# Optimization experiments

Hardware: AMD Instinct MI355X
Metric: run time of the kernel (lower is better)

## Reference

```python
import jax, jax.numpy as jnp
import numpy as np

B, LIMG, LTXT = 1, 2048, 256
H, NH, HD = 3072, 24, 128
MLP = int(H * 4.0)
EPS = 1e-6


def setup_inputs() -> dict:
    key = jax.random.key(0)
    ks = iter(jax.random.split(key, 64))
    rn = lambda shape, s=0.02: jax.random.normal(next(ks), shape, jnp.float32) * s
    inp = {
        'img': jax.random.normal(next(ks), (B, LIMG, H), jnp.float32),
        'txt': jax.random.normal(next(ks), (B, LTXT, H), jnp.float32),
        'vec': jax.random.normal(next(ks), (B, H), jnp.float32),
        'pe': jax.random.normal(next(ks), (1, 1, LTXT + LIMG, HD // 2, 2, 2), jnp.float32),
    }
    for p in ('img', 'txt'):
        inp[f'{p}_mod_w'] = rn((H, 6 * H)); inp[f'{p}_mod_b'] = jnp.zeros((6 * H,), jnp.float32)
        inp[f'{p}_ln1_s'] = jnp.ones((H,), jnp.float32); inp[f'{p}_ln1_b'] = jnp.zeros((H,), jnp.float32)
        inp[f'{p}_qkv_w'] = rn((H, 3 * H)); inp[f'{p}_qkv_b'] = jnp.zeros((3 * H,), jnp.float32)
        inp[f'{p}_qn'] = jnp.ones((HD,), jnp.float32); inp[f'{p}_kn'] = jnp.ones((HD,), jnp.float32)
        inp[f'{p}_proj_w'] = rn((H, H)); inp[f'{p}_proj_b'] = jnp.zeros((H,), jnp.float32)
        inp[f'{p}_ln2_s'] = jnp.ones((H,), jnp.float32); inp[f'{p}_ln2_b'] = jnp.zeros((H,), jnp.float32)
        inp[f'{p}_mlp_w1'] = rn((H, MLP)); inp[f'{p}_mlp_b1'] = jnp.zeros((MLP,), jnp.float32)
        inp[f'{p}_mlp_w2'] = rn((MLP, H)); inp[f'{p}_mlp_b2'] = jnp.zeros((H,), jnp.float32)
    return inp


def _ln(x, s, b):
    m = jnp.mean(x, -1, keepdims=True)
    v = jnp.mean((x - m) ** 2, -1, keepdims=True)
    return (x - m) * jax.lax.rsqrt(v + EPS) * s + b


def _rms(x, s):
    return x * jax.lax.rsqrt(jnp.mean(x * x, -1, keepdims=True) + EPS) * s


def _apply_rope(x, pe):
    # x: (B,NH,L,HD); pe: (1,1,L,HD/2,2,2)
    xr = x.reshape(*x.shape[:-1], HD // 2, 1, 2)
    out = pe[..., 0] * xr[..., 0] + pe[..., 1] * xr[..., 1]  # (B,NH,L,HD/2,2)
    return out.reshape(x.shape)


def _attention(q, k, v, pe):
    q = _apply_rope(q, pe)
    k = _apply_rope(k, pe)
    scores = jnp.einsum('bhqd,bhkd->bhqk', q, k) / jnp.sqrt(jnp.float32(HD))
    a = jax.nn.softmax(scores, axis=-1)
    x = jnp.einsum('bhqk,bhkd->bhqd', a, v)  # (B,NH,L,HD)
    return x.transpose(0, 2, 1, 3).reshape(x.shape[0], x.shape[2], NH * HD)


def _mod(vec, w, b):
    o = jnp.dot(jax.nn.silu(vec), w) + b          # (B, 6H)
    return jnp.split(o[:, None, :], 6, axis=-1)


def _qkv_heads(x, w, b, qn, kn):
    Bx, L, _ = x.shape
    qkv = (jnp.dot(x, w) + b).reshape(Bx, L, 3, NH, HD).transpose(2, 0, 3, 1, 4)
    q, k, v = qkv[0], qkv[1], qkv[2]
    return _rms(q, qn), _rms(k, kn), v


def reference(img, txt, vec, pe,
              img_mod_w, img_mod_b, img_ln1_s, img_ln1_b, img_qkv_w, img_qkv_b,
              img_qn, img_kn, img_proj_w, img_proj_b, img_ln2_s, img_ln2_b,
              img_mlp_w1, img_mlp_b1, img_mlp_w2, img_mlp_b2,
              txt_mod_w, txt_mod_b, txt_ln1_s, txt_ln1_b, txt_qkv_w, txt_qkv_b,
              txt_qn, txt_kn, txt_proj_w, txt_proj_b, txt_ln2_s, txt_ln2_b,
              txt_mlp_w1, txt_mlp_b1, txt_mlp_w2, txt_mlp_b2):
    i_sh1, i_sc1, i_g1, i_sh2, i_sc2, i_g2 = _mod(vec, img_mod_w, img_mod_b)
    t_sh1, t_sc1, t_g1, t_sh2, t_sc2, t_g2 = _mod(vec, txt_mod_w, txt_mod_b)

    img_mod = (1 + i_sc1) * _ln(img, img_ln1_s, img_ln1_b) + i_sh1
    txt_mod = (1 + t_sc1) * _ln(txt, txt_ln1_s, txt_ln1_b) + t_sh1

    iq, ik, iv = _qkv_heads(img_mod, img_qkv_w, img_qkv_b, img_qn, img_kn)
    tq, tk, tv = _qkv_heads(txt_mod, txt_qkv_w, txt_qkv_b, txt_qn, txt_kn)

    q = jnp.concatenate([tq, iq], axis=2)
    k = jnp.concatenate([tk, ik], axis=2)
    v = jnp.concatenate([tv, iv], axis=2)
    attn = _attention(q, k, v, pe)  # (B, Ltxt+Limg, H)
    Lt = txt.shape[1]
    txt_attn, img_attn = attn[:, :Lt], attn[:, Lt:]

    img = img + i_g1 * (jnp.dot(img_attn, img_proj_w) + img_proj_b)
    h = (1 + i_sc2) * _ln(img, img_ln2_s, img_ln2_b) + i_sh2
    img = img + i_g2 * (jnp.dot(jax.nn.gelu(jnp.dot(h, img_mlp_w1) + img_mlp_b1), img_mlp_w2) + img_mlp_b2)

    txt = txt + t_g1 * (jnp.dot(txt_attn, txt_proj_w) + txt_proj_b)
    h = (1 + t_sc2) * _ln(txt, txt_ln2_s, txt_ln2_b) + t_sh2
    txt = txt + t_g2 * (jnp.dot(jax.nn.gelu(jnp.dot(h, txt_mlp_w1) + txt_mlp_b1), txt_mlp_w2) + txt_mlp_b2)
    return (img, txt)
```

## Files before the change

### kernel.cpp

```cpp
#include <hip/hip_runtime.h>
#include <hip/hip_bf16.h>
#include <cstdint>

typedef __attribute__((ext_vector_type(8))) short s16x8;
typedef __attribute__((ext_vector_type(4))) short s16x4;
typedef __attribute__((ext_vector_type(2))) short s16x2;
typedef __attribute__((ext_vector_type(4))) float f32x4;

#define LTXT 256
#define LIMG 2048
#define LTOT 2304
#define HDIM 3072
#define NHEADS 24
#define HD 128
#define MLPD 12288

__device__ __forceinline__ short f2bf(float f) {
  union { float f; uint32_t u; } v; v.f = f;
  uint32_t r = v.u + 0x7FFFu + ((v.u >> 16) & 1u);
  return (short)(r >> 16);
}
__device__ __forceinline__ float bf2f(short s) {
  union { uint32_t u; float f; } v; v.u = ((uint32_t)(uint16_t)s) << 16;
  return v.f;
}

#define GLDS16(gsrc, ldst)                                                   \
  __builtin_amdgcn_global_load_lds(                                          \
      (const __attribute__((address_space(1))) uint32_t*)(gsrc),             \
      (__attribute__((address_space(3))) uint32_t*)(ldst), 16, 0, 0)

__global__ __launch_bounds__(256)
void wconv(const float* __restrict__ Wf, short* __restrict__ Wt, int K, int N)
{
  __shared__ short Ls[64][68];
  const int t = threadIdx.x;
  const int k0 = blockIdx.x * 64, n0 = blockIdx.y * 64;
  #pragma unroll
  for (int rep = 0; rep < 4; ++rep) {
    int idx = rep * 256 + t;
    int k = idx >> 4;
    int n = (idx & 15) * 4;
    float4 v = *(const float4*)(Wf + (size_t)(k0 + k) * N + n0 + n);
    Ls[k][n + 0] = f2bf(v.x); Ls[k][n + 1] = f2bf(v.y);
    Ls[k][n + 2] = f2bf(v.z); Ls[k][n + 3] = f2bf(v.w);
  }
  __syncthreads();
  #pragma unroll
  for (int rep = 0; rep < 4; ++rep) {
    int idx = rep * 256 + t;
    int n = idx >> 4;
    int k = (idx & 15) * 4;
    s16x4 o = { Ls[k + 0][n], Ls[k + 1][n], Ls[k + 2][n], Ls[k + 3][n] };
    *(s16x4*)(Wt + (size_t)(n0 + n) * K + k0 + k) = o;
  }
}

__global__ __launch_bounds__(256)
void mod_gemv(const float* __restrict__ vec,
              const float* __restrict__ w_img, const float* __restrict__ b_img,
              const float* __restrict__ w_txt, const float* __restrict__ b_txt,
              float* __restrict__ mod_img, float* __restrict__ mod_txt)
{
  __shared__ float sv[HDIM];
  const int t = threadIdx.x;
  for (int i = t; i < HDIM; i += 256) {
    float x = vec[i];
    sv[i] = x / (1.f + __expf(-x));
  }
  __syncthreads();
  const float* w = blockIdx.y ? w_txt : w_img;
  const float* bb = blockIdx.y ? b_txt : b_img;
  float* o = blockIdx.y ? mod_txt : mod_img;
  const int lane = t & 63, kc = t >> 6;
  const int colbase = blockIdx.x * 256 + lane * 4;
  f32x4 acc = {0.f, 0.f, 0.f, 0.f};
  const float* wp = w + (size_t)kc * 768 * 18432 + colbase;
  #pragma unroll 4
  for (int k = 0; k < 768; ++k) {
    float4 wv = *(const float4*)wp;
    float s = sv[kc * 768 + k];
    acc[0] += s * wv.x; acc[1] += s * wv.y;
    acc[2] += s * wv.z; acc[3] += s * wv.w;
    wp += 18432;
  }
  __shared__ f32x4 part[4][64];
  part[kc][lane] = acc;
  __syncthreads();
  if (t < 64) {
    f32x4 r = part[0][t];
    #pragma unroll
    for (int c = 1; c < 4; ++c) r += part[c][t];
    int cb = blockIdx.x * 256 + t * 4;
    float4 bv = *(const float4*)(bb + cb);
    float4 ov; ov.x = r[0] + bv.x; ov.y = r[1] + bv.y;
    ov.z = r[2] + bv.z; ov.w = r[3] + bv.w;
    *(float4*)(o + cb) = ov;
  }
}

__global__ __launch_bounds__(256)
void ln_mod(const float* __restrict__ xi, const float* __restrict__ xt, int rows_img,
            const float* __restrict__ si, const float* __restrict__ bi,
            const float* __restrict__ st, const float* __restrict__ bt,
            const float* __restrict__ modi, const float* __restrict__ modt,
            int sh_chunk, int sc_chunk,
            short* __restrict__ oi, short* __restrict__ ot)
{
  const int row = blockIdx.x;
  const float *x, *s, *b, *mod;
  short* out;
  if (row < rows_img) {
    x = xi + (size_t)row * HDIM; s = si; b = bi; mod = modi;
    out = oi + (size_t)row * HDIM;
  } else {
    int lr = row - rows_img;
    x = xt + (size_t)lr * HDIM; s = st; b = bt; mod = modt;
    out = ot + (size_t)lr * HDIM;
  }
  const float* sh = mod + (size_t)sh_chunk * HDIM;
  const float* sc = mod + (size_t)sc_chunk * HDIM;
  const int t = threadIdx.x;
  float xv[12];
  {
    float4 a = *(const float4*)(x + t * 12 + 0);
    float4 c = *(const float4*)(x + t * 12 + 4);
    float4 d = *(const float4*)(x + t * 12 + 8);
    xv[0]=a.x; xv[1]=a.y; xv[2]=a.z; xv[3]=a.w;
    xv[4]=c.x; xv[5]=c.y; xv[6]=c.z; xv[7]=c.w;
    xv[8]=d.x; xv[9]=d.y; xv[10]=d.z; xv[11]=d.w;
  }
  float sum = 0.f, ss = 0.f;
  #pragma unroll
  for (int e = 0; e < 12; ++e) { sum += xv[e]; ss += xv[e] * xv[e]; }
  for (int xm = 1; xm < 64; xm <<= 1) {
    sum += __shfl_xor(sum, xm);
    ss  += __shfl_xor(ss, xm);
  }
  __shared__ float red[8];
  const int w = t >> 6, lane = t & 63;
  if (lane == 0) { red[w] = sum; red[4 + w] = ss; }
  __syncthreads();
  sum = red[0] + red[1] + red[2] + red[3];
  ss  = red[4] + red[5] + red[6] + red[7];
  const float mean = sum * (1.f / HDIM);
  const float var = ss * (1.f / HDIM) - mean * mean;
  const float rs = rsqrtf(var + 1e-6f);
  short ov[12];
  #pragma unroll
  for (int e = 0; e < 12; ++e) {
    int c = t * 12 + e;
    float y = (xv[e] - mean) * rs * s[c] + b[c];
    ov[e] = f2bf((1.f + sc[c]) * y + sh[c]);
  }
  #pragma unroll
  for (int j = 0; j < 3; ++j) {
    s16x4 v = { ov[j*4+0], ov[j*4+1], ov[j*4+2], ov[j*4+3] };
    *(s16x4*)(out + t * 12 + j * 4) = v;
  }
}

template<int EPI>
__global__ __launch_bounds__(512, 2)
void gemm256(const short* __restrict__ A, int K, int N, int split,
             const short* __restrict__ W0, const short* __restrict__ W1,
             const float* __restrict__ b0, const float* __restrict__ b1,
             void* __restrict__ out0, void* __restrict__ out1,
             const float* __restrict__ r0, const float* __restrict__ r1,
             const float* __restrict__ g0, const float* __restrict__ g1)
{
  __shared__ __align__(16) short lds[65536];
  const int tid = threadIdx.x;
  const int lane = tid & 63, w = tid >> 6;
  const int wm = w >> 2, wn = w & 3;
  const int l15 = lane & 15, lg = lane >> 4;

  const int gx = gridDim.x;
  const int nwg = gx * gridDim.y;
  const int lin = blockIdx.y * gx + blockIdx.x;
  const int q8 = nwg >> 3, r8 = nwg & 7;
  const int xcd = lin & 7, loc = lin >> 3;
  const int nid = (xcd < r8 ? xcd * (q8 + 1) : r8 * (q8 + 1) + (xcd - r8) * q8) + loc;
  const int bm = nid % gx, bn = nid / gx;

  const bool is1 = bm >= split;
  const int m0 = bm * 256, n0 = bn * 256;
  const short* WT = is1 ? W1 : W0;
  const float* bias = is1 ? b1 : b0;
  const int nt = K >> 6;

  f32x4 acc[8][4];
  #pragma unroll
  for (int i = 0; i < 8; ++i)
    #pragma unroll
    for (int j = 0; j < 4; ++j)
      acc[i][j] = f32x4{0.f, 0.f, 0.f, 0.f};

  auto stage_item = [&](const short* mat, int grow0, int tt, int kh, int ldsOff) {
    const int kb = tt * 64 + kh * 32;
    #pragma unroll
    for (int l = 0; l < 2; ++l) {
      const int chrow = w * 32 + l * 16 + (lane >> 2);
      const int lc = (lane & 3) ^ ((chrow >> 1) & 3);
      GLDS16(mat + (size_t)(grow0 + chrow) * K + kb + lc * 8,
             lds + ldsOff + (w * 2 + l) * 512);
    }
  };

  const int rA0 = wm * 128 + l15;
  const int rB0 = wn * 64 + l15;
  const int cofs = (lg ^ ((l15 >> 1) & 3)) * 8;

  s16x8 av[4], bv[4];
  auto ldA4 = [&](int c, int ks, int mfb) {
    const short* base = lds + c * 32768 + ks * 8192;
    #pragma unroll
    for (int i = 0; i < 4; ++i)
      av[i] = *(const s16x8*)(base + (rA0 + (mfb + i) * 16) * 32 + cofs);
  };
  auto ldB4 = [&](int c, int ks) {
    const short* base = lds + c * 32768 + 16384 + ks * 8192;
    #pragma unroll
    for (int i = 0; i < 4; ++i)
      bv[i] = *(const s16x8*)(base + (rB0 + i * 16) * 32 + cofs);
  };
  auto quad = [&](int mfb) {
    __builtin_amdgcn_s_setprio(1);
    #pragma unroll
    for (int i = 0; i < 4; ++i)
      #pragma unroll
      for (int j = 0; j < 4; ++j)
        acc[mfb + i][j] = __builtin_amdgcn_mfma_f32_16x16x32_bf16(
            av[i], bv[j], acc[mfb + i][j], 0, 0, 0);
    __builtin_amdgcn_s_setprio(0);
  };

  stage_item(A, m0, 0, 0, 0);
  stage_item(WT, n0, 0, 0, 16384);
  stage_item(A, m0, 0, 1, 8192);
  stage_item(WT, n0, 0, 1, 24576);
  if (nt > 1) {
    stage_item(A, m0, 1, 0, 32768);
    stage_item(WT, n0, 1, 0, 49152);
  }
  asm volatile("s_waitcnt vmcnt(8)" ::: "memory");
  __builtin_amdgcn_s_barrier();
  __builtin_amdgcn_sched_barrier(0);

  for (int t = 0; t < nt; ++t) {
    const int c = t & 1;
    const int cb = c * 32768, cnb = (c ^ 1) * 32768;
    ldA4(c, 0, 0);
    ldB4(c, 0);
    if (t + 1 < nt) stage_item(A, m0, t + 1, 1, cnb + 8192);
    __builtin_amdgcn_s_barrier();
    __builtin_amdgcn_sched_barrier(0);
    quad(0);
    __builtin_amdgcn_s_barrier();
    __builtin_amdgcn_sched_barrier(0);
    ldA4(c, 0, 4);
    if (t + 1 < nt) {
      stage_item(WT, n0, t + 1, 1, cnb + 24576);
      asm volatile("s_waitcnt vmcnt(8)" ::: "memory");
    } else {
      asm volatile("s_waitcnt vmcnt(0)" ::: "memory");
    }
    __builtin_amdgcn_s_barrier();
    __builtin_amdgcn_sched_barrier(0);
    quad(4);
    __builtin_amdgcn_s_barrier();
    __builtin_amdgcn_sched_barrier(0);
    ldA4(c, 1, 0);
    ldB4(c, 1);
    if (t + 2 < nt) stage_item(A, m0, t + 2, 0, cb);
    __builtin_amdgcn_s_barrier();
    __builtin_amdgcn_sched_barrier(0);
    quad(0);
    __builtin_amdgcn_s_barrier();
    __builtin_amdgcn_sched_barrier(0);
    ldA4(c, 1, 4);
    if (t + 2 < nt) {
      stage_item(WT, n0, t + 2, 0, cb + 16384);
      asm volatile("s_waitcnt vmcnt(8)" ::: "memory");
    } else if (t + 1 < nt) {
      asm volatile("s_waitcnt vmcnt(4)" ::: "memory");
    }
    __builtin_amdgcn_s_barrier();
    __builtin_amdgcn_sched_barrier(0);
    quad(4);
    __builtin_amdgcn_s_barrier();
    __builtin_amdgcn_sched_barrier(0);
  }

  const int lrbase = m0 - (is1 ? split * 256 : 0);
  #pragma unroll
  for (int mf = 0; mf < 8; ++mf)
    #pragma unroll
    for (int nf = 0; nf < 4; ++nf) {
      int col = n0 + wn * 64 + nf * 16 + l15;
      float bvs = bias[col];
      #pragma unroll
      for (int r = 0; r < 4; ++r) {
        int row = lrbase + wm * 128 + mf * 16 + lg * 4 + r;
        float x = acc[mf][nf][r] + bvs;
        if constexpr (EPI == 0) {
          short* o = (short*)(is1 ? out1 : out0);
          o[(size_t)row * N + col] = f2bf(x);
        } else if constexpr (EPI == 1) {
          float g = 0.5f * x * (1.f + tanhf(0.7978845608028654f * (x + 0.044715f * x * x * x)));
          short* o = (short*)(is1 ? out1 : out0);
          o[(size_t)row * N + col] = f2bf(g);
        } else if constexpr (EPI == 2) {
          const float* resid = is1 ? r1 : r0;
          const float* gate = is1 ? g1 : g0;
          float* o = (float*)(is1 ? out1 : out0);
          o[(size_t)row * N + col] = resid[(size_t)row * N + col] + gate[col] * x;
        } else {
          const float* gate = is1 ? g1 : g0;
          float* o = (float*)(is1 ? out1 : out0);
          size_t ix = (size_t)row * N + col;
          o[ix] = o[ix] + gate[col] * x;
        }
      }
    }
}

__global__ __launch_bounds__(256)
void qkvr(const short* __restrict__ qkv, const float* __restrict__ pe,
          const float* __restrict__ qn_img, const float* __restrict__ kn_img,
          const float* __restrict__ qn_txt, const float* __restrict__ kn_txt,
          short* __restrict__ Qh, short* __restrict__ Kh)
{
  const int w = threadIdx.x >> 6, lane = threadIdx.x & 63;
  const int tok = blockIdx.x * 4 + w;
  const int h = blockIdx.y;
  const float* qn = (tok < LTXT) ? qn_txt : qn_img;
  const float* kn = (tok < LTXT) ? kn_txt : kn_img;
  const size_t base = (size_t)tok * 9216 + (size_t)h * HD + lane * 2;
  const float4 p4 = *(const float4*)(pe + ((size_t)tok * 64 + lane) * 4);
  {
    s16x2 qs = *(const s16x2*)(qkv + base);
    float x0 = bf2f(qs[0]), x1 = bf2f(qs[1]);
    float sq = x0 * x0 + x1 * x1;
    for (int xm = 1; xm < 64; xm <<= 1) sq += __shfl_xor(sq, xm);
    float r = rsqrtf(sq * (1.f / HD) + 1e-6f);
    x0 = x0 * r * qn[lane * 2]; x1 = x1 * r * qn[lane * 2 + 1];
    s16x2 o = { f2bf(p4.x * x0 + p4.y * x1), f2bf(p4.z * x0 + p4.w * x1) };
    *(s16x2*)(Qh + ((size_t)h * LTOT + tok) * HD + lane * 2) = o;
  }
  {
    s16x2 ks = *(const s16x2*)(qkv + base + HDIM);
    float x0 = bf2f(ks[0]), x1 = bf2f(ks[1]);
    float sq = x0 * x0 + x1 * x1;
    for (int xm = 1; xm < 64; xm <<= 1) sq += __shfl_xor(sq, xm);
    float r = rsqrtf(sq * (1.f / HD) + 1e-6f);
    x0 = x0 * r * kn[lane * 2]; x1 = x1 * r * kn[lane * 2 + 1];
    s16x2 o = { f2bf(p4.x * x0 + p4.y * x1), f2bf(p4.z * x0 + p4.w * x1) };
    *(s16x2*)(Kh + ((size_t)h * LTOT + tok) * HD + lane * 2) = o;
  }
}

__global__ __launch_bounds__(256)
void vt_k(const short* __restrict__ qkv, short* __restrict__ VT)
{
  __shared__ __align__(16) short Vs[64][136];
  const int h = blockIdx.y, tok0 = blockIdx.x * 64;
  const int t = threadIdx.x;
  #pragma unroll
  for (int rep = 0; rep < 4; ++rep) {
    int idx = rep * 256 + t;
    int tk = idx >> 4, oct = idx & 15;
    *(s16x8*)(&Vs[tk][oct * 8]) =
        *(const s16x8*)(qkv + (size_t)(tok0 + tk) * 9216 + 6144 + (size_t)h * HD + oct * 8);
  }
  __syncthreads();
  #pragma unroll
  for (int rep = 0; rep < 4; ++rep) {
    int idx = rep * 256 + t;
    int d = idx >> 3, tg = idx & 7;
    s16x8 o;
    #pragma unroll
    for (int j = 0; j < 8; ++j) o[j] = Vs[tg * 8 + j][d];
    *(s16x8*)(VT + ((size_t)h * HD + d) * LTOT + tok0 + tg * 8) = o;
  }
}

__global__ __launch_bounds__(256, 2)
void attn_k(const short* __restrict__ Qh, const short* __restrict__ Kh,
            const short* __restrict__ VT, short* __restrict__ out)
{
  __shared__ __align__(16) short Ps[4][32][72];
  const int t = threadIdx.x, lane = t & 63, w = t >> 6;
  const int l15 = lane & 15, lg = lane >> 4;
  const int h = blockIdx.y;
  const int qrow = blockIdx.x * 128 + w * 32;

  s16x8 qf[2][4];
  #pragma unroll
  for (int mf = 0; mf < 2; ++mf)
    #pragma unroll
    for (int ks = 0; ks < 4; ++ks)
      qf[mf][ks] = *(const s16x8*)(Qh + ((size_t)h * LTOT + qrow + mf * 16 + l15) * HD + ks * 32 + lg * 8);

  f32x4 O[2][8];
  #pragma unroll
  for (int mf = 0; mf < 2; ++mf)
    #pragma unroll
    for (int dt = 0; dt < 8; ++dt) O[mf][dt] = f32x4{0.f, 0.f, 0.f, 0.f};
  float mrow[2][4], lrow[2][4];
  #pragma unroll
  for (int mf = 0; mf < 2; ++mf)
    #pragma unroll
    for (int r = 0; r < 4; ++r) { mrow[mf][r] = -1e30f; lrow[mf][r] = 0.f; }

  for (int kt = 0; kt < LTOT / 64; ++kt) {
    const int k0 = kt * 64;
    f32x4 S[2][4];
    #pragma unroll
    for (int mf = 0; mf < 2; ++mf)
      #pragma unroll
      for (int jt = 0; jt < 4; ++jt) S[mf][jt] = f32x4{0.f, 0.f, 0.f, 0.f};
    #pragma unroll
    for (int ks = 0; ks < 4; ++ks)
      #pragma unroll
      for (int jt = 0; jt < 4; ++jt) {
        s16x8 kf = *(const s16x8*)(Kh + ((size_t)h * LTOT + k0 + jt * 16 + l15) * HD + ks * 32 + lg * 8);
        S[0][jt] = __builtin_amdgcn_mfma_f32_16x16x32_bf16(qf[0][ks], kf, S[0][jt], 0, 0, 0);
        S[1][jt] = __builtin_amdgcn_mfma_f32_16x16x32_bf16(qf[1][ks], kf, S[1][jt], 0, 0, 0);
      }
    #pragma unroll
    for (int mf = 0; mf < 2; ++mf) {
      const float scl = 0.08838834764831845f;
      #pragma unroll
      for (int jt = 0; jt < 4; ++jt) S[mf][jt] *= scl;
      float pm[4];
      #pragma unroll
      for (int r = 0; r < 4; ++r)
        pm[r] = fmaxf(fmaxf(S[mf][0][r], S[mf][1][r]), fmaxf(S[mf][2][r], S[mf][3][r]));
      for (int xm = 1; xm < 16; xm <<= 1)
        #pragma unroll
        for (int r = 0; r < 4; ++r) pm[r] = fmaxf(pm[r], __shfl_xor(pm[r], xm));
      f32x4 corrv;
      #pragma unroll
      for (int r = 0; r < 4; ++r) {
        float mn = fmaxf(mrow[mf][r], pm[r]);
        corrv[r] = __expf(mrow[mf][r] - mn);
        mrow[mf][r] = mn;
      }
      float rs[4] = {0.f, 0.f, 0.f, 0.f};
      #pragma unroll
      for (int jt = 0; jt < 4; ++jt)
        #pragma unroll
        for (int r = 0; r < 4; ++r) {
          float p = __expf(S[mf][jt][r] - mrow[mf][r]);
          S[mf][jt][r] = p;
          rs[r] += p;
        }
      for (int xm = 1; xm < 16; xm <<= 1)
        #pragma unroll
        for (int r = 0; r < 4; ++r) rs[r] += __shfl_xor(rs[r], xm);
      #pragma unroll
      for (int r = 0; r < 4; ++r) lrow[mf][r] = lrow[mf][r] * corrv[r] + rs[r];
      #pragma unroll
      for (int dt = 0; dt < 8; ++dt) O[mf][dt] *= corrv;
      #pragma unroll
      for (int jt = 0; jt < 4; ++jt)
        #pragma unroll
        for (int r = 0; r < 4; ++r)
          Ps[w][mf * 16 + lg * 4 + r][jt * 16 + l15] = f2bf(S[mf][jt][r]);
    }
    asm volatile("s_waitcnt lgkmcnt(0)" ::: "memory");
    __builtin_amdgcn_sched_barrier(0);
    #pragma unroll
    for (int kk2 = 0; kk2 < 2; ++kk2) {
      s16x8 pf0 = *(const s16x8*)(&Ps[w][l15][kk2 * 32 + lg * 8]);
      s16x8 pf1 = *(const s16x8*)(&Ps[w][16 + l15][kk2 * 32 + lg * 8]);
      #pragma unroll
      for (int dt = 0; dt < 8; ++dt) {
        s16x8 vf = *(const s16x8*)(VT + ((size_t)h * HD + dt * 16 + l15) * LTOT + k0 + kk2 * 32 + lg * 8);
        O[0][dt] = __builtin_amdgcn_mfma_f32_16x16x32_bf16(pf0, vf, O[0][dt], 0, 0, 0);
        O[1][dt] = __builtin_amdgcn_mfma_f32_16x16x32_bf16(pf1, vf, O[1][dt], 0, 0, 0);
      }
    }
    asm volatile("s_waitcnt lgkmcnt(0)" ::: "memory");
    __builtin_amdgcn_sched_barrier(0);
  }
  #pragma unroll
  for (int mf = 0; mf < 2; ++mf) {
    f32x4 inv;
    #pragma unroll
    for (int r = 0; r < 4; ++r) inv[r] = 1.f / lrow[mf][r];
    #pragma unroll
    for (int dt = 0; dt < 8; ++dt) {
      f32x4 o = O[mf][dt] * inv;
      #pragma unroll
      for (int r = 0; r < 4; ++r)
        out[(size_t)(qrow + mf * 16 + lg * 4 + r) * HDIM + (size_t)h * HD + dt * 16 + l15] = f2bf(o[r]);
    }
  }
}

extern "C" void kernel_launch(void* const* d_in, const int* in_sizes, int n_in,
                              void* d_out, int out_size, void* d_ws, size_t ws_size,
                              hipStream_t stream)
{
  (void)in_sizes; (void)n_in; (void)out_size;
  const float* img = (const float*)d_in[0];
  const float* txt = (const float*)d_in[1];
  const float* vec = (const float*)d_in[2];
  const float* pe  = (const float*)d_in[3];
  const float* Pi[16]; const float* Pt[16];
  for (int i = 0; i < 16; ++i) Pi[i] = (const float*)d_in[4 + i];
  for (int i = 0; i < 16; ++i) Pt[i] = (const float*)d_in[20 + i];

  char* ws = (char*)d_ws;
  float* MODI = (float*)(ws + 0);
  float* MODT = (float*)(ws + 73728);
  short* XMI  = (short*)(ws + 147456);
  short* XMT  = (short*)(ws + 12730368);
  short* QKV  = (short*)(ws + 14303232);
  short* QHh  = (short*)(ws + 56770560);
  short* KHh  = (short*)(ws + 70926336);
  short* VTt  = (short*)(ws + 85082112);
  short* ATT  = (short*)(ws + 99237888);
  short* H1   = (short*)(ws + 14303232);
  short* WTA  = (short*)(ws + 113393664);
  short* WTB  = (short*)(ws + 188891136);
  if (ws_size < (size_t)264388608) return;
  float* outI = (float*)d_out;
  float* outT = outI + (size_t)LIMG * HDIM;

  mod_gemv<<<dim3(72, 2), 256, 0, stream>>>(vec, Pi[0], Pi[1], Pt[0], Pt[1], MODI, MODT);
  ln_mod<<<dim3(LTOT), 256, 0, stream>>>(img, txt, LIMG, Pi[2], Pi[3], Pt[2], Pt[3],
                                         MODI, MODT, 0, 1, XMI, XMT);
  wconv<<<dim3(48, 144), 256, 0, stream>>>(Pi[4], WTA, HDIM, 3 * HDIM);
  wconv<<<dim3(48, 144), 256, 0, stream>>>(Pt[4], WTB, HDIM, 3 * HDIM);
  gemm256<0><<<dim3(9, 36), 512, 0, stream>>>(XMI, HDIM, 3 * HDIM, 8,
      WTA, WTB, Pi[5], Pt[5],
      QKV + (size_t)LTXT * 9216, QKV, nullptr, nullptr, nullptr, nullptr);
  qkvr<<<dim3(LTOT / 4, NHEADS), 256, 0, stream>>>(QKV, pe, Pi[6], Pi[7], Pt[6], Pt[7], QHh, KHh);
  vt_k<<<dim3(LTOT / 64, NHEADS), 256, 0, stream>>>(QKV, VTt);
  attn_k<<<dim3(LTOT / 128, NHEADS), 256, 0, stream>>>(QHh, KHh, VTt, ATT);
  wconv<<<dim3(48, 48), 256, 0, stream>>>(Pt[8], WTA, HDIM, HDIM);
  wconv<<<dim3(48, 48), 256, 0, stream>>>(Pi[8], WTB, HDIM, HDIM);
  gemm256<2><<<dim3(9, 12), 512, 0, stream>>>(ATT, HDIM, HDIM, 1,
      WTA, WTB, Pt[9], Pi[9], outT, outI, txt, img,
      MODT + 2 * HDIM, MODI + 2 * HDIM);
  ln_mod<<<dim3(LTOT), 256, 0, stream>>>(outI, outT, LIMG, Pi[10], Pi[11], Pt[10], Pt[11],
                                         MODI, MODT, 3, 4, XMI, XMT);
  wconv<<<dim3(48, 192), 256, 0, stream>>>(Pi[12], WTA, HDIM, MLPD);
  wconv<<<dim3(48, 192), 256, 0, stream>>>(Pt[12], WTB, HDIM, MLPD);
  gemm256<1><<<dim3(9, 48), 512, 0, stream>>>(XMI, HDIM, MLPD, 8,
      WTA, WTB, Pi[13], Pt[13],
      H1, H1 + (size_t)LIMG * MLPD, nullptr, nullptr, nullptr, nullptr);
  wconv<<<dim3(192, 48), 256, 0, stream>>>(Pi[14], WTA, MLPD, HDIM);
  wconv<<<dim3(192, 48), 256, 0, stream>>>(Pt[14], WTB, MLPD, HDIM);
  gemm256<3><<<dim3(9, 12), 512, 0, stream>>>(H1, MLPD, HDIM, 8,
      WTA, WTB, Pi[15], Pt[15], outI, outT, nullptr, nullptr,
      MODI + 5 * HDIM, MODT + 5 * HDIM);
}
```

Measured before the change: 1.545 ms.

## Restructure GEMM main loop: load all A fragments, split B halves, reorder prefetch

The bf16 GEMM inner loop now loads all eight A fragments per k-step and splits B into two halves of two fragments, instead of four A and four B per quad. The global-to-LDS prefetch order is reshuffled so three sub-tiles are in flight before the loop. Near the tail it uses a 'deep' flag that switches to a full vmcnt(0) wait, and the sched_barrier calls are removed. The goal is to cut LDS reloads of B and overlap more global loads with MFMA work. In exchange it holds more A registers, which risks register pressure, and the unconditional prologue staging assumes nt>1.

```diff
diff --git a/kernel.cpp b/kernel.cpp
--- a/kernel.cpp
+++ b/kernel.cpp
@@ -211,27 +211,27 @@
   const int rB0 = wn * 64 + l15;
   const int cofs = (lg ^ ((l15 >> 1) & 3)) * 8;
 
-  s16x8 av[4], bv[4];
-  auto ldA4 = [&](int c, int ks, int mfb) {
+  s16x8 av[8], bv[2];
+  auto ldAV = [&](int c, int ks) {
     const short* base = lds + c * 32768 + ks * 8192;
     #pragma unroll
-    for (int i = 0; i < 4; ++i)
-      av[i] = *(const s16x8*)(base + (rA0 + (mfb + i) * 16) * 32 + cofs);
+    for (int i = 0; i < 8; ++i)
+      av[i] = *(const s16x8*)(base + (rA0 + i * 16) * 32 + cofs);
   };
-  auto ldB4 = [&](int c, int ks) {
+  auto ldBV = [&](int c, int ks, int nh) {
     const short* base = lds + c * 32768 + 16384 + ks * 8192;
     #pragma unroll
-    for (int i = 0; i < 4; ++i)
-      bv[i] = *(const s16x8*)(base + (rB0 + i * 16) * 32 + cofs);
+    for (int j = 0; j < 2; ++j)
+      bv[j] = *(const s16x8*)(base + (rB0 + (nh * 2 + j) * 16) * 32 + cofs);
   };
-  auto quad = [&](int mfb) {
+  auto mfma16 = [&](int nh) {
     __builtin_amdgcn_s_setprio(1);
     #pragma unroll
-    for (int i = 0; i < 4; ++i)
-      #pragma unroll
-      for (int j = 0; j < 4; ++j)
-        acc[mfb + i][j] = __builtin_amdgcn_mfma_f32_16x16x32_bf16(
-            av[i], bv[j], acc[mfb + i][j], 0, 0, 0);
+    for (int i = 0; i < 8; ++i)
+      #pragma unroll
+      for (int j = 0; j < 2; ++j)
+        acc[i][nh * 2 + j] = __builtin_amdgcn_mfma_f32_16x16x32_bf16(
+            av[i], bv[j], acc[i][nh * 2 + j], 0, 0, 0);
     __builtin_amdgcn_s_setprio(0);
   };
 
@@ -239,57 +239,42 @@
   stage_item(WT, n0, 0, 0, 16384);
   stage_item(A, m0, 0, 1, 8192);
   stage_item(WT, n0, 0, 1, 24576);
-  if (nt > 1) {
-    stage_item(A, m0, 1, 0, 32768);
-    stage_item(WT, n0, 1, 0, 49152);
-  }
-  asm volatile("s_waitcnt vmcnt(8)" ::: "memory");
+  stage_item(A, m0, 1, 0, 32768);
+  stage_item(WT, n0, 1, 0, 49152);
+  stage_item(A, m0, 1, 1, 40960);
+  asm volatile("s_waitcnt vmcnt(10)" ::: "memory");
   __builtin_amdgcn_s_barrier();
-  __builtin_amdgcn_sched_barrier(0);
 
   for (int t = 0; t < nt; ++t) {
     const int c = t & 1;
     const int cb = c * 32768, cnb = (c ^ 1) * 32768;
-    ldA4(c, 0, 0);
-    ldB4(c, 0);
-    if (t + 1 < nt) stage_item(A, m0, t + 1, 1, cnb + 8192);
-    __builtin_amdgcn_s_barrier();
-    __builtin_amdgcn_sched_barrier(0);
-    quad(0);
-    __builtin_amdgcn_s_barrier();
-    __builtin_amdgcn_sched_barrier(0);
-    ldA4(c, 0, 4);
-    if (t + 1 < nt) {
-      stage_item(WT, n0, t + 1, 1, cnb + 24576);
-      asm volatile("s_waitcnt vmcnt(8)" ::: "memory");
-    } else {
-      asm volatile("s_waitcnt vmcnt(0)" ::: "memory");
-    }
-    __builtin_amdgcn_s_barrier();
-    __builtin_amdgcn_sched_barrier(0);
-    quad(4);
-    __builtin_amdgcn_s_barrier();
-    __builtin_amdgcn_sched_barrier(0);
-    ldA4(c, 1, 0);
-    ldB4(c, 1);
+    const bool deep = (t < nt - 3);
+    ldAV(c, 0);
+    ldBV(c, 0, 0);
+    if (t + 1 < nt) stage_item(WT, n0, t + 1, 1, cnb + 24576);
+    __builtin_amdgcn_s_barrier();
+    mfma16(0);
+    __builtin_amdgcn_s_barrier();
+    ldBV(c, 0, 1);
     if (t + 2 < nt) stage_item(A, m0, t + 2, 0, cb);
-    __builtin_amdgcn_s_barrier();
-    __builtin_amdgcn_sched_barrier(0);
-    quad(0);
-    __builtin_amdgcn_s_barrier();
-    __builtin_amdgcn_sched_barrier(0);
-    ldA4(c, 1, 4);
-    if (t + 2 < nt) {
-      stage_item(WT, n0, t + 2, 0, cb + 16384);
-      asm volatile("s_waitcnt vmcnt(8)" ::: "memory");
-    } else if (t + 1 < nt) {
-      asm volatile("s_waitcnt vmcnt(4)" ::: "memory");
-    }
-    __builtin_amdgcn_s_barrier();
-    __builtin_amdgcn_sched_barrier(0);
-    quad(4);
-    __builtin_amdgcn_s_barrier();
-    __builtin_amdgcn_sched_barrier(0);
+    if (deep) asm volatile("s_waitcnt vmcnt(8)" ::: "memory");
+    else      asm volatile("s_waitcnt vmcnt(0)" ::: "memory");
+    __builtin_amdgcn_s_barrier();
+    mfma16(1);
+    __builtin_amdgcn_s_barrier();
+    ldAV(c, 1);
+    ldBV(c, 1, 0);
+    if (t + 2 < nt) stage_item(WT, n0, t + 2, 0, cb + 16384);
+    __builtin_amdgcn_s_barrier();
+    mfma16(0);
+    __builtin_amdgcn_s_barrier();
+    ldBV(c, 1, 1);
+    if (t + 2 < nt) stage_item(A, m0, t + 2, 1, cb + 8192);
+    if (deep) asm volatile("s_waitcnt vmcnt(8)" ::: "memory");
+    else      asm volatile("s_waitcnt vmcnt(0)" ::: "memory");
+    __builtin_amdgcn_s_barrier();
+    mfma16(1);
+    __builtin_amdgcn_s_barrier();
   }
 
   const int lrbase = m0 - (is1 ? split * 256 : 0);
```

Result: no change. 1.567 ms (+1.4%).
